# Kernel optimization log

Hardware: AMD Instinct MI355X
Metric: run time of the kernel (lower is better)

Reference implementation:

```python
import jax, jax.numpy as jnp
import numpy as np

B, LQ, LK, D, H = 4, 1024, 1024, 512, 8


def setup_inputs() -> dict:
    key = jax.random.key(0)
    ks = jax.random.split(key, 6)
    # xavier_normal for (D, D): std = sqrt(2 / (D + D))
    std_qkv = (2.0 / (D + D)) ** 0.5
    std_p = (2.0 / (H * D + D)) ** 0.5
    x = jax.random.normal(ks[0], (B, LQ, D), dtype=jnp.float32)
    states = jax.random.normal(ks[1], (B, LK, D), dtype=jnp.float32)
    mask = jnp.ones((B, LQ, LK), dtype=jnp.int32)
    # per-head full-size QKV weights, stacked over heads: [H, D, D]
    Wq = jax.random.normal(ks[2], (H, D, D), dtype=jnp.float32) * std_qkv
    Wk = jax.random.normal(ks[3], (H, D, D), dtype=jnp.float32) * std_qkv
    Wv = jax.random.normal(ks[4], (H, D, D), dtype=jnp.float32) * std_qkv
    Wp = jax.random.normal(ks[5], (D, H * D), dtype=jnp.float32) * std_p
    return {"x": x, "states": states, "mask": mask,
            "Wq": Wq, "Wk": Wk, "Wv": Wv, "Wp": Wp}


def reference(x, states, mask, Wq, Wk, Wv, Wp):
    # Per-head linear projections (nn.Linear: y = x @ W.T), batched over heads.
    q = jnp.einsum('bld,hed->bhle', x, Wq)        # [B,H,Lq,D]
    k = jnp.einsum('bsd,hed->bhse', states, Wk)   # [B,H,Lk,D]
    v = jnp.einsum('bsd,hed->bhse', states, Wv)   # [B,H,Lk,D]
    scale = 1.0 / (D ** 0.5)
    scores = jnp.einsum('bhle,bhse->bhls', q, k) * scale  # [B,H,Lq,Lk]
    scores = jnp.where(mask[:, None, :, :] == 0, -jnp.inf, scores)
    attn = jax.nn.softmax(scores, axis=-1)
    # Original does broadcast multiply + sum; mathematically this is attn @ v.
    ctx = jnp.einsum('bhls,bhse->bhle', attn, v)  # [B,H,Lq,D]
    # torch.cat over heads in order -> head-major last dim
    ctx = jnp.transpose(ctx, (0, 2, 1, 3)).reshape(B, LQ, H * D)
    return ctx @ Wp.T  # [B,Lq,D]
```

## Files before the change

### kernel.cpp

```cpp
#include <hip/hip_runtime.h>
#include <hip/hip_bf16.h>
#include <cstdint>
#include <cstddef>


typedef __bf16 bf16;
typedef __bf16 bf16x4 __attribute__((ext_vector_type(4)));
typedef __bf16 bf16x8 __attribute__((ext_vector_type(8)));
typedef float f32x4 __attribute__((ext_vector_type(4)));

__device__ inline void gload_lds16(const void* g, void* l) {
  __builtin_amdgcn_global_load_lds(
      (const __attribute__((address_space(1))) void*)g,
      (__attribute__((address_space(3))) void*)l, 16, 0, 0);
}

template <typename CT, int MODE>
__device__ __forceinline__ void gemm_body(
    bf16* As, bf16* Bs,
    const bf16* __restrict__ A, const bf16* __restrict__ B, CT* __restrict__ C,
    int K, int lda, int ldb, int ldc, int m0, int n0, float scale,
    const unsigned* __restrict__ mrow, float* __restrict__ sumrow)
{
  const int t = threadIdx.x;
  const int lane = t & 63, w = t >> 6;
  const int wm = w >> 1, wn = w & 1;

  const int srow = t >> 3;
  const int schunk = (t & 7) ^ (srow & 7);
  const bf16* Ag = A + (size_t)(m0 + srow) * lda + schunk * 8;
  const bf16* Bg = B + (size_t)(n0 + srow) * ldb + schunk * 8;
  bf16* Als = As + t * 8;
  bf16* Bls = Bs + t * 8;

  f32x4 acc[4][4] = {};
  const int rr = lane & 15;
  const int q4 = lane >> 4;

  const int kIters = K >> 6;
  for (int kt = 0; kt < kIters; ++kt) {
    __syncthreads();
#pragma unroll
    for (int i = 0; i < 4; ++i) {
      gload_lds16(Ag + (size_t)(32 * i) * lda, Als + i * 2048);
      gload_lds16(Bg + (size_t)(32 * i) * ldb, Bls + i * 2048);
    }
    Ag += 64; Bg += 64;
    __syncthreads();

#pragma unroll
    for (int kk = 0; kk < 2; ++kk) {
      bf16x8 af[4], bfr[4];
      const int ck = kk * 4 + q4;
#pragma unroll
      for (int r = 0; r < 4; ++r) {
        const int R = wm * 64 + r * 16 + rr;
        af[r] = *(const bf16x8*)(As + R * 64 + ((ck ^ (R & 7)) << 3));
      }
#pragma unroll
      for (int c = 0; c < 4; ++c) {
        const int R = wn * 64 + c * 16 + rr;
        bfr[c] = *(const bf16x8*)(Bs + R * 64 + ((ck ^ (R & 7)) << 3));
      }
#pragma unroll
      for (int r = 0; r < 4; ++r)
#pragma unroll
        for (int c = 0; c < 4; ++c)
          acc[r][c] = __builtin_amdgcn_mfma_f32_16x16x32_bf16(af[r], bfr[c], acc[r][c], 0, 0, 0);
    }
  }

  if (MODE == 0) {
#pragma unroll
    for (int r = 0; r < 4; ++r) {
#pragma unroll
      for (int c = 0; c < 4; ++c) {
        const int gr0 = m0 + wm * 64 + r * 16 + (q4 << 2);
        const int gc = n0 + wn * 64 + c * 16 + rr;
#pragma unroll
        for (int i = 0; i < 4; ++i)
          C[(size_t)(gr0 + i) * ldc + gc] = (CT)(acc[r][c][i] * scale);
      }
    }
  } else {
    const int cb0 = (n0 + wn * 64) >> 5;
#pragma unroll
    for (int r = 0; r < 4; ++r) {
#pragma unroll
      for (int i = 0; i < 4; ++i) {
        const int row = m0 + wm * 64 + r * 16 + (q4 << 2) + i;
        const unsigned mw0 = mrow[(row << 5) + cb0];
        const unsigned mw1 = mrow[(row << 5) + cb0 + 1];
        float ps = 0.0f;
#pragma unroll
        for (int c = 0; c < 4; ++c) {
          const int gc = n0 + wn * 64 + c * 16 + rr;
          const unsigned mw = (c >= 2) ? mw1 : mw0;
          const unsigned bit = (mw >> (((c & 1) << 4) + rr)) & 1u;
          float p = bit ? __expf(acc[r][c][i] * scale) : 0.0f;
          C[(size_t)row * ldc + gc] = (CT)p;
          ps += p;
        }
        ps += __shfl_xor(ps, 1); ps += __shfl_xor(ps, 2);
        ps += __shfl_xor(ps, 4); ps += __shfl_xor(ps, 8);
        if (rr == 0) atomicAdd(sumrow + row, ps);
      }
    }
  }
}

__global__ __launch_bounds__(256) void prep_kernel(
    const float* __restrict__ x, const float* __restrict__ st,
    const float* __restrict__ Wq, const float* __restrict__ Wk,
    const float* __restrict__ Wp, const float* __restrict__ Wv,
    const int* __restrict__ mask,
    bf16* __restrict__ xb, bf16* __restrict__ stb, bf16* __restrict__ wqb,
    bf16* __restrict__ wkb, bf16* __restrict__ wpb, bf16* __restrict__ WvT,
    unsigned* __restrict__ mbits, float* __restrict__ sums)
{
  const int lin = blockIdx.x;
  const int t = threadIdx.x;
  if (lin < 10240) {
    const float* s; bf16* d;
    switch (lin >> 11) {
      case 0: s = x; d = xb; break;
      case 1: s = st; d = stb; break;
      case 2: s = Wq; d = wqb; break;
      case 3: s = Wk; d = wkb; break;
      default: s = Wp; d = wpb; break;
    }
    const int i = ((lin & 2047) * 256 + t) * 4;
    float4 v = *(const float4*)(s + i);
    bf16x4 o;
    o[0] = (bf16)v.x; o[1] = (bf16)v.y; o[2] = (bf16)v.z; o[3] = (bf16)v.w;
    *(bf16x4*)(d + i) = o;
  } else if (lin < 12288) {
    const int gid = (lin - 10240) * 256 + t;
    const int e0 = (gid & 127) * 4;
    const int d = (gid >> 7) & 511;
    const int h = gid >> 16;
    const float* src = Wv + (size_t)h * 262144 + (size_t)e0 * 512 + d;
    bf16x4 o;
    o[0] = (bf16)src[0];
    o[1] = (bf16)src[512];
    o[2] = (bf16)src[1024];
    o[3] = (bf16)src[1536];
    *(bf16x4*)(WvT + (size_t)h * 262144 + (size_t)d * 512 + e0) = o;
  } else if (lin < 12800) {
    const int gid = (lin - 12288) * 256 + t;
    const int* src = mask + (size_t)gid * 32;
    unsigned bits = 0;
#pragma unroll
    for (int j = 0; j < 32; j += 4) {
      int4 v = *(const int4*)(src + j);
      if (v.x) bits |= 1u << j;
      if (v.y) bits |= 1u << (j + 1);
      if (v.z) bits |= 1u << (j + 2);
      if (v.w) bits |= 1u << (j + 3);
    }
    mbits[gid] = bits;
  } else {
    const int i = ((lin - 12800) * 256 + t) * 4;
    *(float4*)(sums + i) = make_float4(0.f, 0.f, 0.f, 0.f);
  }
}

__global__ __launch_bounds__(256) void proj_kernel(
    const bf16* __restrict__ xb, const bf16* __restrict__ stb,
    const bf16* __restrict__ wqb, const bf16* __restrict__ wkb,
    const bf16* __restrict__ wpb, const bf16* __restrict__ WvT,
    bf16* __restrict__ q, bf16* __restrict__ k, bf16* __restrict__ U)
{
  __shared__ bf16 As[128 * 64];
  __shared__ bf16 Bs[128 * 64];
  const int lin = blockIdx.x;
  if (lin < 2048) {
    const int g = ((lin >> 8) << 3) | (lin & 7);
    const int tile = (lin >> 3) & 31;
    const int job = g >> 5;
    const int zz = g & 31;
    const size_t zb = zz >> 3, zh = zz & 7;
    const bf16* Ain = (job == 0) ? xb : stb;
    const bf16* W = (job == 0) ? wqb : wkb;
    bf16* Cout = (job == 0) ? q : k;
    gemm_body<bf16, 0>(As, Bs, Ain + zb * 524288, W + zh * 262144,
        Cout + zb * 4194304 + zh * 524288, 512, 512, 512, 512,
        (tile >> 2) * 128, (tile & 3) * 128, 1.0f, nullptr, nullptr);
  } else {
    const int lin2 = lin - 2048;
    const int h = lin2 >> 4;
    const int tile = lin2 & 15;
    gemm_body<bf16, 0>(As, Bs, wpb + (size_t)h * 512, WvT + (size_t)h * 262144,
        U + (size_t)h * 262144, 512, 4096, 512, 512,
        (tile >> 2) * 128, (tile & 3) * 128, 1.0f, nullptr, nullptr);
  }
}

__global__ __launch_bounds__(256) void big_kernel(
    const bf16* __restrict__ q, const bf16* __restrict__ k,
    const bf16* __restrict__ U, const bf16* __restrict__ stb,
    bf16* __restrict__ P, bf16* __restrict__ VWT,
    const unsigned* __restrict__ mbits, float* __restrict__ sums, float scale)
{
  __shared__ bf16 As[128 * 64];
  __shared__ bf16 Bs[128 * 64];
  const int lin = blockIdx.x;
  if (lin < 2048) {
    const int z = ((lin >> 9) << 3) | (lin & 7);
    const int j = (lin >> 3) & 63;
    const int zb = z >> 3, zh = z & 7;
    const bf16* A = q + (size_t)zb * 4194304 + (size_t)zh * 524288;
    const bf16* B = k + (size_t)zb * 4194304 + (size_t)zh * 524288;
    bf16* C = P + (size_t)zb * 8388608 + (size_t)zh * 1048576;
    const unsigned* mrow = mbits + ((size_t)zb << 15);
    float* sumrow = sums + ((size_t)z << 10);
    gemm_body<bf16, 1>(As, Bs, A, B, C, 512, 512, 512, 1024,
                       (j >> 3) * 128, (j & 7) * 128, scale, mrow, sumrow);
  } else {
    const int lin2 = lin - 2048;
    const int z = ((lin2 >> 8) << 3) | (lin2 & 7);
    const int j = (lin2 >> 3) & 31;
    const int zb = z >> 3, zh = z & 7;
    gemm_body<bf16, 0>(As, Bs, U + (size_t)zh * 262144, stb + (size_t)zb * 524288,
        VWT + (size_t)zb * 4194304 + (size_t)zh * 524288, 512, 512, 512, 1024,
        (j >> 3) * 128, (j & 7) * 128, 1.0f, nullptr, nullptr);
  }
}

__global__ __launch_bounds__(256) void pvw_kernel(
    const bf16* __restrict__ P, const bf16* __restrict__ VWT,
    const float* __restrict__ sums, float* __restrict__ part)
{
  __shared__ bf16 As[128 * 64];
  __shared__ bf16 Bs[128 * 64];
  const int lin = blockIdx.x;
  const int z = ((lin >> 8) << 3) | (lin & 7);
  const int j = (lin >> 3) & 31;
  const int zb = z >> 2, hp = z & 3;
  const int m0 = (j >> 2) * 128, n0 = (j & 3) * 128;
  const int t = threadIdx.x;
  const int lane = t & 63, w = t >> 6;
  const int wm = w >> 1, wn = w & 1;
  const int srow = t >> 3, schunk = (t & 7) ^ (srow & 7);
  const int rr = lane & 15, q4 = lane >> 4;
  bf16* Als = As + t * 8;
  bf16* Bls = Bs + t * 8;

  f32x4 accO[4][4] = {};

#pragma unroll
  for (int hh = 0; hh < 2; ++hh) {
    const int h = hp * 2 + hh;
    const bf16* Ag = P + (size_t)zb * 8388608 + (size_t)h * 1048576
                       + (size_t)(m0 + srow) * 1024 + schunk * 8;
    const bf16* Bg = VWT + (size_t)zb * 4194304 + (size_t)h * 524288
                        + (size_t)(n0 + srow) * 1024 + schunk * 8;
    f32x4 acc[4][4] = {};
    for (int kt = 0; kt < 16; ++kt) {
      __syncthreads();
#pragma unroll
      for (int i = 0; i < 4; ++i) {
        gload_lds16(Ag + (size_t)(32 * i) * 1024, Als + i * 2048);
        gload_lds16(Bg + (size_t)(32 * i) * 1024, Bls + i * 2048);
      }
      Ag += 64; Bg += 64;
      __syncthreads();
#pragma unroll
      for (int kk = 0; kk < 2; ++kk) {
        bf16x8 af[4], bfr[4];
        const int ck = kk * 4 + q4;
#pragma unroll
        for (int r = 0; r < 4; ++r) {
          const int R = wm * 64 + r * 16 + rr;
          af[r] = *(const bf16x8*)(As + R * 64 + ((ck ^ (R & 7)) << 3));
        }
#pragma unroll
        for (int c = 0; c < 4; ++c) {
          const int R = wn * 64 + c * 16 + rr;
          bfr[c] = *(const bf16x8*)(Bs + R * 64 + ((ck ^ (R & 7)) << 3));
        }
#pragma unroll
        for (int r = 0; r < 4; ++r)
#pragma unroll
          for (int c = 0; c < 4; ++c)
            acc[r][c] = __builtin_amdgcn_mfma_f32_16x16x32_bf16(af[r], bfr[c], acc[r][c], 0, 0, 0);
      }
    }
    const float* srs = sums + ((size_t)zb * 8 + h) * 1024;
#pragma unroll
    for (int r = 0; r < 4; ++r) {
#pragma unroll
      for (int i = 0; i < 4; ++i) {
        const float inv = 1.0f / srs[m0 + wm * 64 + r * 16 + (q4 << 2) + i];
#pragma unroll
        for (int c = 0; c < 4; ++c)
          accO[r][c][i] += acc[r][c][i] * inv;
      }
    }
  }

  float* Cp = part + (size_t)hp * 2097152 + (size_t)zb * 524288;
#pragma unroll
  for (int r = 0; r < 4; ++r) {
#pragma unroll
    for (int c = 0; c < 4; ++c) {
      const int gr0 = m0 + wm * 64 + r * 16 + (q4 << 2);
      const int gc = n0 + wn * 64 + c * 16 + rr;
#pragma unroll
      for (int i = 0; i < 4; ++i)
        Cp[(size_t)(gr0 + i) * 512 + gc] = accO[r][c][i];
    }
  }
}

__global__ __launch_bounds__(256) void reduce4(
    const float* __restrict__ part, float* __restrict__ out)
{
  const size_t i = ((size_t)blockIdx.x * 256 + threadIdx.x) * 4;
  float4 a = *(const float4*)(part + i);
  float4 b = *(const float4*)(part + 2097152 + i);
  float4 c = *(const float4*)(part + 4194304 + i);
  float4 d = *(const float4*)(part + 6291456 + i);
  float4 o;
  o.x = (a.x + b.x) + (c.x + d.x);
  o.y = (a.y + b.y) + (c.y + d.y);
  o.z = (a.z + b.z) + (c.z + d.z);
  o.w = (a.w + b.w) + (c.w + d.w);
  *(float4*)(out + i) = o;
}

extern "C" void kernel_launch(void* const* d_in, const int* in_sizes, int n_in,
                              void* d_out, int out_size, void* d_ws, size_t ws_size,
                              hipStream_t stream) {
  const float* x    = (const float*)d_in[0];
  const float* st   = (const float*)d_in[1];
  const int*   mask = (const int*)d_in[2];
  const float* Wq   = (const float*)d_in[3];
  const float* Wk   = (const float*)d_in[4];
  const float* Wv   = (const float*)d_in[5];
  const float* Wp   = (const float*)d_in[6];
  float* out = (float*)d_out;

  char* ws = (char*)d_ws;
  const size_t MB = 1048576;
  bf16* xb  = (bf16*)(ws);
  bf16* stb = (bf16*)(ws + 4 * MB);
  bf16* wqb = (bf16*)(ws + 8 * MB);
  bf16* wkb = (bf16*)(ws + 12 * MB);
  bf16* wpb = (bf16*)(ws + 16 * MB);
  bf16* WvT = (bf16*)(ws + 20 * MB);
  bf16* U   = (bf16*)(ws + 24 * MB);
  bf16* q   = (bf16*)(ws + 28 * MB);
  bf16* k   = (bf16*)(ws + 60 * MB);
  bf16* VWT = (bf16*)(ws + 92 * MB);
  bf16* sc  = (bf16*)(ws + 124 * MB);
  unsigned* mbits = (unsigned*)(ws + 188 * MB);
  float*    sums  = (float*)(ws + 189 * MB);
  float*    part  = (float*)(ws + 28 * MB);

  dim3 blk(256);
  const float scale = 0.04419417382415922f;

  prep_kernel<<<dim3(12832), blk, 0, stream>>>(x, st, Wq, Wk, Wp, Wv, mask,
      xb, stb, wqb, wkb, wpb, WvT, mbits, sums);

  proj_kernel<<<dim3(2176), blk, 0, stream>>>(xb, stb, wqb, wkb, wpb, WvT,
      q, k, U);

  big_kernel<<<dim3(3072), blk, 0, stream>>>(q, k, U, stb, sc, VWT,
      mbits, sums, scale);

  pvw_kernel<<<dim3(512), blk, 0, stream>>>(sc, VWT, sums, part);

  reduce4<<<dim3(2048), blk, 0, stream>>>(part, out);
}
```

Measured before the change: 277.3 us.

## Switch GEMMs to 256x256 tiles with 4-stage async LDS pipeline and 8-wave blocks

Replaces the 128x128 single-buffered GEMM body with a 256x256-tile, 512-thread version that prefetches three K-slices ahead into a 4-deep LDS ring, using explicit vmcnt waits, barriers and setprio around the MFMA blocks. All GEMM kernels are relaunched with fewer, larger blocks and XCD-aware block index remapping. The PV kernel now handles one head per block with normalisation in the epilogue, writing 8 partials that reduce8 sums instead of 4. The aim is to hide global-load latency and raise data reuse per tile. In exchange it uses 128KB of LDS per block and launches fewer blocks, while the partial buffer and the final reduction double in size.

```diff
diff --git a/kernel.cpp b/kernel.cpp
--- a/kernel.cpp
+++ b/kernel.cpp
@@ -16,94 +16,149 @@
 }
 
 template <typename CT, int MODE>
-__device__ __forceinline__ void gemm_body(
-    bf16* As, bf16* Bs,
+__device__ __forceinline__ void gemm256(
+    bf16* lds,
     const bf16* __restrict__ A, const bf16* __restrict__ B, CT* __restrict__ C,
     int K, int lda, int ldb, int ldc, int m0, int n0, float scale,
     const unsigned* __restrict__ mrow, float* __restrict__ sumrow)
 {
   const int t = threadIdx.x;
-  const int lane = t & 63, w = t >> 6;
-  const int wm = w >> 1, wn = w & 1;
-
-  const int srow = t >> 3;
-  const int schunk = (t & 7) ^ (srow & 7);
-  const bf16* Ag = A + (size_t)(m0 + srow) * lda + schunk * 8;
-  const bf16* Bg = B + (size_t)(n0 + srow) * ldb + schunk * 8;
-  bf16* Als = As + t * 8;
-  bf16* Bls = Bs + t * 8;
-
-  f32x4 acc[4][4] = {};
-  const int rr = lane & 15;
-  const int q4 = lane >> 4;
-
-  const int kIters = K >> 6;
-  for (int kt = 0; kt < kIters; ++kt) {
-    __syncthreads();
-#pragma unroll
-    for (int i = 0; i < 4; ++i) {
-      gload_lds16(Ag + (size_t)(32 * i) * lda, Als + i * 2048);
-      gload_lds16(Bg + (size_t)(32 * i) * ldb, Bls + i * 2048);
-    }
-    Ag += 64; Bg += 64;
-    __syncthreads();
-
-#pragma unroll
-    for (int kk = 0; kk < 2; ++kk) {
-      bf16x8 af[4], bfr[4];
-      const int ck = kk * 4 + q4;
-#pragma unroll
-      for (int r = 0; r < 4; ++r) {
-        const int R = wm * 64 + r * 16 + rr;
-        af[r] = *(const bf16x8*)(As + R * 64 + ((ck ^ (R & 7)) << 3));
+  const int lane = t & 63;
+  const int w = t >> 6;
+  const int wm = w >> 2, wn = w & 3;
+  const int rr = lane & 15, q4 = lane >> 4;
+
+  const int tr = t >> 2;
+  const int tc = (t & 3) ^ (tr & 3);
+  const bf16* Ag = A + (size_t)(m0 + tr) * lda + tc * 8;
+  const bf16* Bg = B + (size_t)(n0 + tr) * ldb + tc * 8;
+  bf16* ldsSt = lds + t * 8;
+
+  const int nT = K >> 5;
+
+  auto stageA = [&](int tt) {
+    bf16* d = ldsSt + (tt & 3) * 16384;
+    const bf16* s = Ag + tt * 32;
+    gload_lds16(s, d);
+    gload_lds16(s + (size_t)128 * lda, d + 4096);
+  };
+  auto stageB = [&](int tt) {
+    bf16* d = ldsSt + (tt & 3) * 16384 + 8192;
+    const bf16* s = Bg + tt * 32;
+    gload_lds16(s, d);
+    gload_lds16(s + (size_t)128 * ldb, d + 4096);
+  };
+
+  stageA(0); stageB(0);
+  stageA(1); stageB(1);
+  stageA(2); stageB(2);
+  asm volatile("s_waitcnt vmcnt(8)" ::: "memory");
+  __builtin_amdgcn_s_barrier();
+  __builtin_amdgcn_sched_barrier(0);
+
+  f32x4 acc[8][4] = {};
+
+  for (int tt = 0; tt < nT; ++tt) {
+    const bf16* Al = lds + (tt & 3) * 16384;
+    const bf16* Bl = Al + 8192;
+    bf16x8 af[4], bg[4];
+
+#pragma unroll
+    for (int m = 0; m < 4; ++m) {
+      const int R = wm * 128 + m * 16 + rr;
+      af[m] = *(const bf16x8*)(Al + R * 32 + ((q4 ^ (R & 3)) << 3));
+    }
+#pragma unroll
+    for (int n = 0; n < 4; ++n) {
+      const int R = wn * 64 + n * 16 + rr;
+      bg[n] = *(const bf16x8*)(Bl + R * 32 + ((q4 ^ (R & 3)) << 3));
+    }
+    if (tt + 3 < nT) stageA(tt + 3);
+    __builtin_amdgcn_s_barrier();
+    __builtin_amdgcn_sched_barrier(0);
+    __builtin_amdgcn_s_setprio(1);
+#pragma unroll
+    for (int m = 0; m < 4; ++m)
+#pragma unroll
+      for (int n = 0; n < 4; ++n)
+        acc[m][n] = __builtin_amdgcn_mfma_f32_16x16x32_bf16(af[m], bg[n], acc[m][n], 0, 0, 0);
+    __builtin_amdgcn_s_setprio(0);
+    __builtin_amdgcn_s_barrier();
+    __builtin_amdgcn_sched_barrier(0);
+
+#pragma unroll
+    for (int m = 0; m < 4; ++m) {
+      const int R = wm * 128 + 64 + m * 16 + rr;
+      af[m] = *(const bf16x8*)(Al + R * 32 + ((q4 ^ (R & 3)) << 3));
+    }
+    if (tt + 3 < nT) stageB(tt + 3);
+    __builtin_amdgcn_s_barrier();
+    __builtin_amdgcn_sched_barrier(0);
+    __builtin_amdgcn_s_setprio(1);
+#pragma unroll
+    for (int m = 0; m < 4; ++m)
+#pragma unroll
+      for (int n = 0; n < 4; ++n)
+        acc[4 + m][n] = __builtin_amdgcn_mfma_f32_16x16x32_bf16(af[m], bg[n], acc[4 + m][n], 0, 0, 0);
+    __builtin_amdgcn_s_setprio(0);
+
+    const int rem = nT - tt;
+    if (rem > 3)       asm volatile("s_waitcnt vmcnt(8)" ::: "memory");
+    else if (rem == 3) asm volatile("s_waitcnt vmcnt(4)" ::: "memory");
+    else               asm volatile("s_waitcnt vmcnt(0)" ::: "memory");
+    __builtin_amdgcn_s_barrier();
+    __builtin_amdgcn_sched_barrier(0);
+  }
+
+  if (MODE == 0) {
+#pragma unroll
+    for (int m = 0; m < 8; ++m) {
+#pragma unroll
+      for (int n = 0; n < 4; ++n) {
+        const int gr0 = m0 + wm * 128 + m * 16 + (q4 << 2);
+        const int gc = n0 + wn * 64 + n * 16 + rr;
+#pragma unroll
+        for (int i = 0; i < 4; ++i)
+          C[(size_t)(gr0 + i) * ldc + gc] = (CT)(acc[m][n][i] * scale);
       }
-#pragma unroll
-      for (int c = 0; c < 4; ++c) {
-        const int R = wn * 64 + c * 16 + rr;
-        bfr[c] = *(const bf16x8*)(Bs + R * 64 + ((ck ^ (R & 7)) << 3));
-      }
-#pragma unroll
-      for (int r = 0; r < 4; ++r)
-#pragma unroll
-        for (int c = 0; c < 4; ++c)
-          acc[r][c] = __builtin_amdgcn_mfma_f32_16x16x32_bf16(af[r], bfr[c], acc[r][c], 0, 0, 0);
-    }
-  }
-
-  if (MODE == 0) {
-#pragma unroll
-    for (int r = 0; r < 4; ++r) {
-#pragma unroll
-      for (int c = 0; c < 4; ++c) {
-        const int gr0 = m0 + wm * 64 + r * 16 + (q4 << 2);
-        const int gc = n0 + wn * 64 + c * 16 + rr;
-#pragma unroll
-        for (int i = 0; i < 4; ++i)
-          C[(size_t)(gr0 + i) * ldc + gc] = (CT)(acc[r][c][i] * scale);
-      }
-    }
-  } else {
+    }
+  } else if (MODE == 1) {
     const int cb0 = (n0 + wn * 64) >> 5;
 #pragma unroll
-    for (int r = 0; r < 4; ++r) {
+    for (int m = 0; m < 8; ++m) {
 #pragma unroll
       for (int i = 0; i < 4; ++i) {
-        const int row = m0 + wm * 64 + r * 16 + (q4 << 2) + i;
+        const int row = m0 + wm * 128 + m * 16 + (q4 << 2) + i;
         const unsigned mw0 = mrow[(row << 5) + cb0];
         const unsigned mw1 = mrow[(row << 5) + cb0 + 1];
         float ps = 0.0f;
 #pragma unroll
-        for (int c = 0; c < 4; ++c) {
-          const int gc = n0 + wn * 64 + c * 16 + rr;
-          const unsigned mw = (c >= 2) ? mw1 : mw0;
-          const unsigned bit = (mw >> (((c & 1) << 4) + rr)) & 1u;
-          float p = bit ? __expf(acc[r][c][i] * scale) : 0.0f;
+        for (int n = 0; n < 4; ++n) {
+          const int gc = n0 + wn * 64 + n * 16 + rr;
+          const unsigned mw = (n >= 2) ? mw1 : mw0;
+          const unsigned bit = (mw >> (((n & 1) << 4) + rr)) & 1u;
+          float p = bit ? __expf(acc[m][n][i] * scale) : 0.0f;
           C[(size_t)row * ldc + gc] = (CT)p;
           ps += p;
         }
         ps += __shfl_xor(ps, 1); ps += __shfl_xor(ps, 2);
         ps += __shfl_xor(ps, 4); ps += __shfl_xor(ps, 8);
         if (rr == 0) atomicAdd(sumrow + row, ps);
+      }
+    }
+  } else {
+#pragma unroll
+    for (int m = 0; m < 8; ++m) {
+      const int gr0 = m0 + wm * 128 + m * 16 + (q4 << 2);
+      float inv[4];
+#pragma unroll
+      for (int i = 0; i < 4; ++i) inv[i] = 1.0f / sumrow[gr0 + i];
+#pragma unroll
+      for (int n = 0; n < 4; ++n) {
+        const int gc = n0 + wn * 64 + n * 16 + rr;
+#pragma unroll
+        for (int i = 0; i < 4; ++i)
+          C[(size_t)(gr0 + i) * ldc + gc] = (CT)(acc[m][n][i] * inv[i]);
       }
     }
   }
@@ -165,167 +220,97 @@
   }
 }
 
-__global__ __launch_bounds__(256) void proj_kernel(
+__global__ __launch_bounds__(512, 2) void proj_kernel(
     const bf16* __restrict__ xb, const bf16* __restrict__ stb,
     const bf16* __restrict__ wqb, const bf16* __restrict__ wkb,
     const bf16* __restrict__ wpb, const bf16* __restrict__ WvT,
     bf16* __restrict__ q, bf16* __restrict__ k, bf16* __restrict__ U)
 {
-  __shared__ bf16 As[128 * 64];
-  __shared__ bf16 Bs[128 * 64];
-  const int lin = blockIdx.x;
-  if (lin < 2048) {
-    const int g = ((lin >> 8) << 3) | (lin & 7);
-    const int tile = (lin >> 3) & 31;
-    const int job = g >> 5;
-    const int zz = g & 31;
+  __shared__ bf16 lds[65536];
+  const int bid = blockIdx.x;
+  const int g = (bid & 7) * 68 + (bid >> 3);
+  if (g < 512) {
+    const int z = g >> 3;
+    const int tile = g & 7;
+    const int job = z >> 5;
+    const int zz = z & 31;
     const size_t zb = zz >> 3, zh = zz & 7;
-    const bf16* Ain = (job == 0) ? xb : stb;
-    const bf16* W = (job == 0) ? wqb : wkb;
-    bf16* Cout = (job == 0) ? q : k;
-    gemm_body<bf16, 0>(As, Bs, Ain + zb * 524288, W + zh * 262144,
+    const bf16* Ain = job ? stb : xb;
+    const bf16* W = job ? wkb : wqb;
+    bf16* Cout = job ? k : q;
+    gemm256<bf16, 0>(lds, Ain + zb * 524288, W + zh * 262144,
         Cout + zb * 4194304 + zh * 524288, 512, 512, 512, 512,
-        (tile >> 2) * 128, (tile & 3) * 128, 1.0f, nullptr, nullptr);
+        (tile >> 1) * 256, (tile & 1) * 256, 1.0f, nullptr, nullptr);
   } else {
-    const int lin2 = lin - 2048;
-    const int h = lin2 >> 4;
-    const int tile = lin2 & 15;
-    gemm_body<bf16, 0>(As, Bs, wpb + (size_t)h * 512, WvT + (size_t)h * 262144,
+    const int g2 = g - 512;
+    const int h = g2 >> 2;
+    const int tile = g2 & 3;
+    gemm256<bf16, 0>(lds, wpb + (size_t)h * 512, WvT + (size_t)h * 262144,
         U + (size_t)h * 262144, 512, 4096, 512, 512,
-        (tile >> 2) * 128, (tile & 3) * 128, 1.0f, nullptr, nullptr);
-  }
-}
-
-__global__ __launch_bounds__(256) void big_kernel(
+        (tile >> 1) * 256, (tile & 1) * 256, 1.0f, nullptr, nullptr);
+  }
+}
+
+__global__ __launch_bounds__(512, 2) void big_kernel(
     const bf16* __restrict__ q, const bf16* __restrict__ k,
     const bf16* __restrict__ U, const bf16* __restrict__ stb,
     bf16* __restrict__ P, bf16* __restrict__ VWT,
     const unsigned* __restrict__ mbits, float* __restrict__ sums, float scale)
 {
-  __shared__ bf16 As[128 * 64];
-  __shared__ bf16 Bs[128 * 64];
-  const int lin = blockIdx.x;
-  if (lin < 2048) {
-    const int z = ((lin >> 9) << 3) | (lin & 7);
-    const int j = (lin >> 3) & 63;
-    const int zb = z >> 3, zh = z & 7;
-    const bf16* A = q + (size_t)zb * 4194304 + (size_t)zh * 524288;
-    const bf16* B = k + (size_t)zb * 4194304 + (size_t)zh * 524288;
-    bf16* C = P + (size_t)zb * 8388608 + (size_t)zh * 1048576;
-    const unsigned* mrow = mbits + ((size_t)zb << 15);
-    float* sumrow = sums + ((size_t)z << 10);
-    gemm_body<bf16, 1>(As, Bs, A, B, C, 512, 512, 512, 1024,
-                       (j >> 3) * 128, (j & 7) * 128, scale, mrow, sumrow);
+  __shared__ bf16 lds[65536];
+  const int bid = blockIdx.x;
+  const int g = (bid & 7) * 96 + (bid >> 3);
+  if (g < 512) {
+    const int z = g >> 4;
+    const int tile = g & 15;
+    const size_t zb = z >> 3, zh = z & 7;
+    gemm256<bf16, 1>(lds,
+        q + zb * 4194304 + zh * 524288,
+        k + zb * 4194304 + zh * 524288,
+        P + zb * 8388608 + zh * 1048576,
+        512, 512, 512, 1024,
+        (tile >> 2) * 256, (tile & 3) * 256, scale,
+        mbits + (zb << 15), sums + ((size_t)z << 10));
   } else {
-    const int lin2 = lin - 2048;
-    const int z = ((lin2 >> 8) << 3) | (lin2 & 7);
-    const int j = (lin2 >> 3) & 31;
-    const int zb = z >> 3, zh = z & 7;
-    gemm_body<bf16, 0>(As, Bs, U + (size_t)zh * 262144, stb + (size_t)zb * 524288,
-        VWT + (size_t)zb * 4194304 + (size_t)zh * 524288, 512, 512, 512, 1024,
-        (j >> 3) * 128, (j & 7) * 128, 1.0f, nullptr, nullptr);
-  }
-}
-
-__global__ __launch_bounds__(256) void pvw_kernel(
+    const int g2 = g - 512;
+    const int z = g2 >> 3;
+    const int tile = g2 & 7;
+    const size_t zb = z >> 3, zh = z & 7;
+    gemm256<bf16, 0>(lds, U + zh * 262144, stb + zb * 524288,
+        VWT + zb * 4194304 + zh * 524288, 512, 512, 512, 1024,
+        (tile >> 2) * 256, (tile & 3) * 256, 1.0f, nullptr, nullptr);
+  }
+}
+
+__global__ __launch_bounds__(512, 2) void pvw_kernel(
     const bf16* __restrict__ P, const bf16* __restrict__ VWT,
-    const float* __restrict__ sums, float* __restrict__ part)
-{
-  __shared__ bf16 As[128 * 64];
-  __shared__ bf16 Bs[128 * 64];
-  const int lin = blockIdx.x;
-  const int z = ((lin >> 8) << 3) | (lin & 7);
-  const int j = (lin >> 3) & 31;
-  const int zb = z >> 2, hp = z & 3;
-  const int m0 = (j >> 2) * 128, n0 = (j & 3) * 128;
-  const int t = threadIdx.x;
-  const int lane = t & 63, w = t >> 6;
-  const int wm = w >> 1, wn = w & 1;
-  const int srow = t >> 3, schunk = (t & 7) ^ (srow & 7);
-  const int rr = lane & 15, q4 = lane >> 4;
-  bf16* Als = As + t * 8;
-  bf16* Bls = Bs + t * 8;
-
-  f32x4 accO[4][4] = {};
-
-#pragma unroll
-  for (int hh = 0; hh < 2; ++hh) {
-    const int h = hp * 2 + hh;
-    const bf16* Ag = P + (size_t)zb * 8388608 + (size_t)h * 1048576
-                       + (size_t)(m0 + srow) * 1024 + schunk * 8;
-    const bf16* Bg = VWT + (size_t)zb * 4194304 + (size_t)h * 524288
-                        + (size_t)(n0 + srow) * 1024 + schunk * 8;
-    f32x4 acc[4][4] = {};
-    for (int kt = 0; kt < 16; ++kt) {
-      __syncthreads();
-#pragma unroll
-      for (int i = 0; i < 4; ++i) {
-        gload_lds16(Ag + (size_t)(32 * i) * 1024, Als + i * 2048);
-        gload_lds16(Bg + (size_t)(32 * i) * 1024, Bls + i * 2048);
-      }
-      Ag += 64; Bg += 64;
-      __syncthreads();
-#pragma unroll
-      for (int kk = 0; kk < 2; ++kk) {
-        bf16x8 af[4], bfr[4];
-        const int ck = kk * 4 + q4;
-#pragma unroll
-        for (int r = 0; r < 4; ++r) {
-          const int R = wm * 64 + r * 16 + rr;
-          af[r] = *(const bf16x8*)(As + R * 64 + ((ck ^ (R & 7)) << 3));
-        }
-#pragma unroll
-        for (int c = 0; c < 4; ++c) {
-          const int R = wn * 64 + c * 16 + rr;
-          bfr[c] = *(const bf16x8*)(Bs + R * 64 + ((ck ^ (R & 7)) << 3));
-        }
-#pragma unroll
-        for (int r = 0; r < 4; ++r)
-#pragma unroll
-          for (int c = 0; c < 4; ++c)
-            acc[r][c] = __builtin_amdgcn_mfma_f32_16x16x32_bf16(af[r], bfr[c], acc[r][c], 0, 0, 0);
-      }
-    }
-    const float* srs = sums + ((size_t)zb * 8 + h) * 1024;
-#pragma unroll
-    for (int r = 0; r < 4; ++r) {
-#pragma unroll
-      for (int i = 0; i < 4; ++i) {
-        const float inv = 1.0f / srs[m0 + wm * 64 + r * 16 + (q4 << 2) + i];
-#pragma unroll
-        for (int c = 0; c < 4; ++c)
-          accO[r][c][i] += acc[r][c][i] * inv;
-      }
-    }
-  }
-
-  float* Cp = part + (size_t)hp * 2097152 + (size_t)zb * 524288;
-#pragma unroll
-  for (int r = 0; r < 4; ++r) {
-#pragma unroll
-    for (int c = 0; c < 4; ++c) {
-      const int gr0 = m0 + wm * 64 + r * 16 + (q4 << 2);
-      const int gc = n0 + wn * 64 + c * 16 + rr;
-#pragma unroll
-      for (int i = 0; i < 4; ++i)
-        Cp[(size_t)(gr0 + i) * 512 + gc] = accO[r][c][i];
-    }
-  }
-}
-
-__global__ __launch_bounds__(256) void reduce4(
+    float* __restrict__ sums, float* __restrict__ part)
+{
+  __shared__ bf16 lds[65536];
+  const int bid = blockIdx.x;
+  const int g = (bid & 7) * 32 + (bid >> 3);
+  const int z = g >> 3;
+  const int tile = g & 7;
+  const size_t zb = z >> 3, zh = z & 7;
+  gemm256<float, 2>(lds,
+      P + zb * 8388608 + zh * 1048576,
+      VWT + zb * 4194304 + zh * 524288,
+      part + zh * 2097152 + zb * 524288,
+      1024, 1024, 1024, 512,
+      (tile >> 1) * 256, (tile & 1) * 256, 1.0f,
+      nullptr, sums + ((size_t)z << 10));
+}
+
+__global__ __launch_bounds__(256) void reduce8(
     const float* __restrict__ part, float* __restrict__ out)
 {
   const size_t i = ((size_t)blockIdx.x * 256 + threadIdx.x) * 4;
-  float4 a = *(const float4*)(part + i);
-  float4 b = *(const float4*)(part + 2097152 + i);
-  float4 c = *(const float4*)(part + 4194304 + i);
-  float4 d = *(const float4*)(part + 6291456 + i);
-  float4 o;
-  o.x = (a.x + b.x) + (c.x + d.x);
-  o.y = (a.y + b.y) + (c.y + d.y);
-  o.z = (a.z + b.z) + (c.z + d.z);
-  o.w = (a.w + b.w) + (c.w + d.w);
+  float4 o = *(const float4*)(part + i);
+#pragma unroll
+  for (int h = 1; h < 8; ++h) {
+    float4 a = *(const float4*)(part + (size_t)h * 2097152 + i);
+    o.x += a.x; o.y += a.y; o.z += a.z; o.w += a.w;
+  }
   *(float4*)(out + i) = o;
 }
 
@@ -358,19 +343,18 @@
   float*    sums  = (float*)(ws + 189 * MB);
   float*    part  = (float*)(ws + 28 * MB);
 
-  dim3 blk(256);
   const float scale = 0.04419417382415922f;
 
-  prep_kernel<<<dim3(12832), blk, 0, stream>>>(x, st, Wq, Wk, Wp, Wv, mask,
+  prep_kernel<<<dim3(12832), dim3(256), 0, stream>>>(x, st, Wq, Wk, Wp, Wv, mask,
       xb, stb, wqb, wkb, wpb, WvT, mbits, sums);
 
-  proj_kernel<<<dim3(2176), blk, 0, stream>>>(xb, stb, wqb, wkb, wpb, WvT,
+  proj_kernel<<<dim3(544), dim3(512), 0, stream>>>(xb, stb, wqb, wkb, wpb, WvT,
       q, k, U);
 
-  big_kernel<<<dim3(3072), blk, 0, stream>>>(q, k, U, stb, sc, VWT,
+  big_kernel<<<dim3(768), dim3(512), 0, stream>>>(q, k, U, stb, sc, VWT,
       mbits, sums, scale);
 
-  pvw_kernel<<<dim3(512), blk, 0, stream>>>(sc, VWT, sums, part);
-
-  reduce4<<<dim3(2048), blk, 0, stream>>>(part, out);
-}
+  pvw_kernel<<<dim3(256), dim3(512), 0, stream>>>(sc, VWT, sums, part);
+
+  reduce8<<<dim3(2048), dim3(256), 0, stream>>>(part, out);
+}
```

New measurement: 333.5 us. +20.3%, slower.

## Fold Wq and Wk into per-head combined matrix to skip K projection

Applied to the files above, without the earlier changes.

Precomputes per-head M = Wq^T Wk (stored transposed) from transposed bf16 weights, then computes tq = x·M and scores = tq·states^T directly, removing the separate K projection GEMM. Q·K^T becomes a GEMM against the shared states rather than per-head k. Splits the old big kernel into a stage2 kernel (tq and V·Wp products) and a scores kernel, adds one launch and a small combine GEMM. Rounding order changes because M is rounded to bf16.

```diff
diff --git a/kernel.cpp b/kernel.cpp
--- a/kernel.cpp
+++ b/kernel.cpp
@@ -111,22 +111,20 @@
 
 __global__ __launch_bounds__(256) void prep_kernel(
     const float* __restrict__ x, const float* __restrict__ st,
-    const float* __restrict__ Wq, const float* __restrict__ Wk,
-    const float* __restrict__ Wp, const float* __restrict__ Wv,
+    const float* __restrict__ Wp, const float* __restrict__ Wq,
+    const float* __restrict__ Wk, const float* __restrict__ Wv,
     const int* __restrict__ mask,
-    bf16* __restrict__ xb, bf16* __restrict__ stb, bf16* __restrict__ wqb,
-    bf16* __restrict__ wkb, bf16* __restrict__ wpb, bf16* __restrict__ WvT,
+    bf16* __restrict__ xb, bf16* __restrict__ stb, bf16* __restrict__ wpb,
+    bf16* __restrict__ WqT, bf16* __restrict__ WkT, bf16* __restrict__ WvT,
     unsigned* __restrict__ mbits, float* __restrict__ sums)
 {
   const int lin = blockIdx.x;
   const int t = threadIdx.x;
-  if (lin < 10240) {
+  if (lin < 6144) {
     const float* s; bf16* d;
     switch (lin >> 11) {
       case 0: s = x; d = xb; break;
       case 1: s = st; d = stb; break;
-      case 2: s = Wq; d = wqb; break;
-      case 3: s = Wk; d = wkb; break;
       default: s = Wp; d = wpb; break;
     }
     const int i = ((lin & 2047) * 256 + t) * 4;
@@ -135,17 +133,24 @@
     o[0] = (bf16)v.x; o[1] = (bf16)v.y; o[2] = (bf16)v.z; o[3] = (bf16)v.w;
     *(bf16x4*)(d + i) = o;
   } else if (lin < 12288) {
-    const int gid = (lin - 10240) * 256 + t;
+    const int tid = lin - 6144;
+    const float* s; bf16* d;
+    switch (tid >> 11) {
+      case 0: s = Wq; d = WqT; break;
+      case 1: s = Wk; d = WkT; break;
+      default: s = Wv; d = WvT; break;
+    }
+    const int gid = (tid & 2047) * 256 + t;
     const int e0 = (gid & 127) * 4;
-    const int d = (gid >> 7) & 511;
+    const int dd = (gid >> 7) & 511;
     const int h = gid >> 16;
-    const float* src = Wv + (size_t)h * 262144 + (size_t)e0 * 512 + d;
+    const float* src = s + (size_t)h * 262144 + (size_t)e0 * 512 + dd;
     bf16x4 o;
     o[0] = (bf16)src[0];
     o[1] = (bf16)src[512];
     o[2] = (bf16)src[1024];
     o[3] = (bf16)src[1536];
-    *(bf16x4*)(WvT + (size_t)h * 262144 + (size_t)d * 512 + e0) = o;
+    *(bf16x4*)(d + (size_t)h * 262144 + (size_t)dd * 512 + e0) = o;
   } else if (lin < 12800) {
     const int gid = (lin - 12288) * 256 + t;
     const int* src = mask + (size_t)gid * 32;
@@ -165,66 +170,74 @@
   }
 }
 
-__global__ __launch_bounds__(256) void proj_kernel(
-    const bf16* __restrict__ xb, const bf16* __restrict__ stb,
-    const bf16* __restrict__ wqb, const bf16* __restrict__ wkb,
+__global__ __launch_bounds__(256) void combine_kernel(
+    const bf16* __restrict__ WqT, const bf16* __restrict__ WkT,
     const bf16* __restrict__ wpb, const bf16* __restrict__ WvT,
-    bf16* __restrict__ q, bf16* __restrict__ k, bf16* __restrict__ U)
+    bf16* __restrict__ Mt, bf16* __restrict__ U)
 {
   __shared__ bf16 As[128 * 64];
   __shared__ bf16 Bs[128 * 64];
-  const int lin = blockIdx.x;
-  if (lin < 2048) {
-    const int g = ((lin >> 8) << 3) | (lin & 7);
-    const int tile = (lin >> 3) & 31;
-    const int job = g >> 5;
-    const int zz = g & 31;
-    const size_t zb = zz >> 3, zh = zz & 7;
-    const bf16* Ain = (job == 0) ? xb : stb;
-    const bf16* W = (job == 0) ? wqb : wkb;
-    bf16* Cout = (job == 0) ? q : k;
-    gemm_body<bf16, 0>(As, Bs, Ain + zb * 524288, W + zh * 262144,
-        Cout + zb * 4194304 + zh * 524288, 512, 512, 512, 512,
+  const int bid = blockIdx.x;
+  const int g = (bid & 7) * 32 + (bid >> 3);
+  const int h = (g >> 4) & 7;
+  const int tile = g & 15;
+  if (g < 128) {
+    gemm_body<bf16, 0>(As, Bs, WkT + (size_t)h * 262144, WqT + (size_t)h * 262144,
+        Mt + (size_t)h * 262144, 512, 512, 512, 512,
         (tile >> 2) * 128, (tile & 3) * 128, 1.0f, nullptr, nullptr);
   } else {
-    const int lin2 = lin - 2048;
-    const int h = lin2 >> 4;
-    const int tile = lin2 & 15;
     gemm_body<bf16, 0>(As, Bs, wpb + (size_t)h * 512, WvT + (size_t)h * 262144,
         U + (size_t)h * 262144, 512, 4096, 512, 512,
         (tile >> 2) * 128, (tile & 3) * 128, 1.0f, nullptr, nullptr);
   }
 }
 
-__global__ __launch_bounds__(256) void big_kernel(
-    const bf16* __restrict__ q, const bf16* __restrict__ k,
-    const bf16* __restrict__ U, const bf16* __restrict__ stb,
-    bf16* __restrict__ P, bf16* __restrict__ VWT,
-    const unsigned* __restrict__ mbits, float* __restrict__ sums, float scale)
+__global__ __launch_bounds__(256) void stage2_kernel(
+    const bf16* __restrict__ xb, const bf16* __restrict__ stb,
+    const bf16* __restrict__ Mt, const bf16* __restrict__ U,
+    bf16* __restrict__ tq, bf16* __restrict__ VWT)
 {
   __shared__ bf16 As[128 * 64];
   __shared__ bf16 Bs[128 * 64];
-  const int lin = blockIdx.x;
-  if (lin < 2048) {
-    const int z = ((lin >> 9) << 3) | (lin & 7);
-    const int j = (lin >> 3) & 63;
-    const int zb = z >> 3, zh = z & 7;
-    const bf16* A = q + (size_t)zb * 4194304 + (size_t)zh * 524288;
-    const bf16* B = k + (size_t)zb * 4194304 + (size_t)zh * 524288;
-    bf16* C = P + (size_t)zb * 8388608 + (size_t)zh * 1048576;
-    const unsigned* mrow = mbits + ((size_t)zb << 15);
-    float* sumrow = sums + ((size_t)z << 10);
-    gemm_body<bf16, 1>(As, Bs, A, B, C, 512, 512, 512, 1024,
-                       (j >> 3) * 128, (j & 7) * 128, scale, mrow, sumrow);
+  const int bid = blockIdx.x;
+  const int g = (bid & 7) * 256 + (bid >> 3);
+  if (g < 1024) {
+    const int z = g >> 5;
+    const int tile = g & 31;
+    const size_t zb = z >> 3, zh = z & 7;
+    gemm_body<bf16, 0>(As, Bs, xb + zb * 524288, Mt + zh * 262144,
+        tq + (size_t)z * 524288, 512, 512, 512, 512,
+        (tile >> 2) * 128, (tile & 3) * 128, 1.0f, nullptr, nullptr);
   } else {
-    const int lin2 = lin - 2048;
-    const int z = ((lin2 >> 8) << 3) | (lin2 & 7);
-    const int j = (lin2 >> 3) & 31;
-    const int zb = z >> 3, zh = z & 7;
-    gemm_body<bf16, 0>(As, Bs, U + (size_t)zh * 262144, stb + (size_t)zb * 524288,
-        VWT + (size_t)zb * 4194304 + (size_t)zh * 524288, 512, 512, 512, 1024,
+    const int g2 = g - 1024;
+    const int z = g2 >> 5;
+    const int j = g2 & 31;
+    const size_t zb = z >> 3, zh = z & 7;
+    gemm_body<bf16, 0>(As, Bs, U + zh * 262144, stb + zb * 524288,
+        VWT + zb * 4194304 + zh * 524288, 512, 512, 512, 1024,
         (j >> 3) * 128, (j & 7) * 128, 1.0f, nullptr, nullptr);
   }
+}
+
+__global__ __launch_bounds__(256) void big_kernel(
+    const bf16* __restrict__ tq, const bf16* __restrict__ stb,
+    bf16* __restrict__ P,
+    const unsigned* __restrict__ mbits, float* __restrict__ sums, float scale)
+{
+  __shared__ bf16 As[128 * 64];
+  __shared__ bf16 Bs[128 * 64];
+  const int bid = blockIdx.x;
+  const int g = (bid & 7) * 256 + (bid >> 3);
+  const int z = g >> 6;
+  const int j = g & 63;
+  const size_t zb = z >> 3, zh = z & 7;
+  gemm_body<bf16, 1>(As, Bs,
+      tq + (size_t)z * 524288,
+      stb + zb * 524288,
+      P + zb * 8388608 + zh * 1048576,
+      512, 512, 512, 1024,
+      (j >> 3) * 128, (j & 7) * 128, scale,
+      mbits + (zb << 15), sums + ((size_t)z << 10));
 }
 
 __global__ __launch_bounds__(256) void pvw_kernel(
@@ -345,30 +358,30 @@
   const size_t MB = 1048576;
   bf16* xb  = (bf16*)(ws);
   bf16* stb = (bf16*)(ws + 4 * MB);
-  bf16* wqb = (bf16*)(ws + 8 * MB);
-  bf16* wkb = (bf16*)(ws + 12 * MB);
-  bf16* wpb = (bf16*)(ws + 16 * MB);
+  bf16* wpb = (bf16*)(ws + 8 * MB);
+  bf16* WqT = (bf16*)(ws + 12 * MB);
+  bf16* WkT = (bf16*)(ws + 16 * MB);
   bf16* WvT = (bf16*)(ws + 20 * MB);
   bf16* U   = (bf16*)(ws + 24 * MB);
-  bf16* q   = (bf16*)(ws + 28 * MB);
-  bf16* k   = (bf16*)(ws + 60 * MB);
-  bf16* VWT = (bf16*)(ws + 92 * MB);
-  bf16* sc  = (bf16*)(ws + 124 * MB);
-  unsigned* mbits = (unsigned*)(ws + 188 * MB);
-  float*    sums  = (float*)(ws + 189 * MB);
-  float*    part  = (float*)(ws + 28 * MB);
+  bf16* Mt  = (bf16*)(ws + 28 * MB);
+  bf16* tq  = (bf16*)(ws + 32 * MB);
+  bf16* VWT = (bf16*)(ws + 64 * MB);
+  bf16* sc  = (bf16*)(ws + 96 * MB);
+  unsigned* mbits = (unsigned*)(ws + 160 * MB);
+  float*    sums  = (float*)(ws + 161 * MB);
+  float*    part  = (float*)(ws + 32 * MB);
 
   dim3 blk(256);
   const float scale = 0.04419417382415922f;
 
-  prep_kernel<<<dim3(12832), blk, 0, stream>>>(x, st, Wq, Wk, Wp, Wv, mask,
-      xb, stb, wqb, wkb, wpb, WvT, mbits, sums);
-
-  proj_kernel<<<dim3(2176), blk, 0, stream>>>(xb, stb, wqb, wkb, wpb, WvT,
-      q, k, U);
-
-  big_kernel<<<dim3(3072), blk, 0, stream>>>(q, k, U, stb, sc, VWT,
-      mbits, sums, scale);
+  prep_kernel<<<dim3(12832), blk, 0, stream>>>(x, st, Wp, Wq, Wk, Wv, mask,
+      xb, stb, wpb, WqT, WkT, WvT, mbits, sums);
+
+  combine_kernel<<<dim3(256), blk, 0, stream>>>(WqT, WkT, wpb, WvT, Mt, U);
+
+  stage2_kernel<<<dim3(2048), blk, 0, stream>>>(xb, stb, Mt, U, tq, VWT);
+
+  big_kernel<<<dim3(2048), blk, 0, stream>>>(tq, stb, sc, mbits, sums, scale);
 
   pvw_kernel<<<dim3(512), blk, 0, stream>>>(sc, VWT, sums, part);
 
```

Result: slower. 284.4 us (+2.5%).
